# Performance work log

Hardware: AMD Instinct MI355X
Metric: run time of the kernel (lower is better)

Reference implementation:

```python
import jax, jax.numpy as jnp
import numpy as np

H, HK, D = 16, 4, 128          # query heads, kv heads, head_dim
HID, INTER = 2048, 8192        # hidden_size, intermediate_size
L, N_UND = 4096, 3072          # total packed len (sum(sample_lens)), num und tokens
SAMPLE_LENS = [2048, 2048]
EPS = 1e-6


def rmsnorm(x, w, eps=EPS):
    v = jnp.mean(jnp.square(x), axis=-1, keepdims=True)
    return x * jax.lax.rsqrt(v + eps) * w


def setup_inputs() -> dict:
    key = jax.random.key(0)
    ks = jax.random.split(key, 12)
    x = jax.random.normal(ks[0], (N_UND, HID), jnp.float32)
    und_idx = jnp.sort(jax.random.permutation(ks[1], L)[:N_UND]).astype(jnp.int64)
    # RoPE tables (source computes RoPE but its attention consumes pre-RoPE tensors)
    pos = jnp.arange(L, dtype=jnp.float32)
    inv_freq = 1.0 / (10000.0 ** (jnp.arange(0, D, 2, dtype=jnp.float32) / D))
    ang = pos[:, None] * inv_freq[None, :]
    cos = jnp.concatenate([jnp.cos(ang), jnp.cos(ang)], axis=-1)
    sin = jnp.concatenate([jnp.sin(ang), jnp.sin(ang)], axis=-1)
    # block-diagonal causal mask over packed sequence (one causal block per sample)
    offs = np.cumsum([0] + SAMPLE_LENS)
    m = np.zeros((L, L), dtype=bool)
    for a, b in zip(offs[:-1], offs[1:]):
        m[a:b, a:b] = np.tril(np.ones((b - a, b - a), dtype=bool))
    mask = jnp.asarray(m)
    w = lambda k, shape: jax.random.normal(k, shape, jnp.float32) * 0.02
    return dict(
        packed_sequence=x, und_idx=und_idx, cos=cos, sin=sin, mask=mask,
        Wq=w(ks[2], (H * D, HID)), bq=w(ks[3], (H * D,)),
        Wk=w(ks[4], (HK * D, HID)), bk=w(ks[5], (HK * D,)),
        Wv=w(ks[6], (HK * D, HID)), bv=w(ks[7], (HK * D,)),
        Wo=w(ks[8], (HID, H * D)),
        q_norm_w=jnp.ones((D,), jnp.float32), k_norm_w=jnp.ones((D,), jnp.float32),
        ln1_w=jnp.ones((HID,), jnp.float32), ln2_w=jnp.ones((HID,), jnp.float32),
        Wg=w(ks[9], (INTER, HID)), Wu=w(ks[10], (INTER, HID)), Wd=w(ks[11], (HID, INTER)),
    )


def reference(packed_sequence, und_idx, cos, sin, mask, Wq, bq, Wk, bk, Wv, bv, Wo,
              q_norm_w, k_norm_w, ln1_w, ln2_w, Wg, Wu, Wd):
    G = H // HK  # num_key_value_groups
    resid = packed_sequence
    x = rmsnorm(packed_sequence, ln1_w)
    # projections on und tokens only, then scatter into zero-initialized packed tensors
    q = (x @ Wq.T + bq).reshape(-1, H, D)
    k = (x @ Wk.T + bk).reshape(-1, HK, D)
    v = (x @ Wv.T + bv).reshape(-1, HK, D)
    Q = jnp.zeros((L, H, D), x.dtype).at[und_idx].set(q)
    K = jnp.zeros((L, HK, D), x.dtype).at[und_idx].set(k)
    V = jnp.zeros((L, HK, D), x.dtype).at[und_idx].set(v)
    # QK RMSNorm (zero rows stay zero, matching scatter-of-normed-und-rows)
    Q = rmsnorm(Q, q_norm_w)
    K = rmsnorm(K, k_norm_w)
    # NOTE: the source applies apply_rotary_pos_emb(Q, K, cos, sin) but both attention
    # branches consume the pre-RoPE normed tensors, so RoPE has no effect; we mirror that.
    Kx = jnp.repeat(K, G, axis=1)  # [L, H, D] GQA expand (each kv head repeated G times)
    Vx = jnp.repeat(V, G, axis=1)
    scores = jnp.einsum('qhd,khd->hqk', Q, Kx) / jnp.sqrt(jnp.asarray(D, x.dtype))
    scores = jnp.where(mask[None], scores, jnp.finfo(scores.dtype).min)
    attn = jax.nn.softmax(scores, axis=-1)
    ctx = jnp.einsum('hqk,khd->qhd', attn, Vx).reshape(L, H * D)
    attn_out = ctx[und_idx] @ Wo.T
    h = resid + attn_out
    y = rmsnorm(h, ln2_w)
    mlp = (jax.nn.silu(y @ Wg.T) * (y @ Wu.T)) @ Wd.T
    return h + mlp
```

## Files before the change

### kernel.cpp

```cpp
#include <hip/hip_runtime.h>
#include <math.h>


#define NU     3072
#define LPACK  4096
#define HIDN   2048
#define QKV_LD 3072
#define EPSF   1e-6f

typedef unsigned short u16;
typedef unsigned int   u32;
typedef unsigned long long u64;
typedef __attribute__((ext_vector_type(8)))  __bf16 bf16x8;
typedef __attribute__((ext_vector_type(4)))  float  f32x4;
typedef __attribute__((ext_vector_type(16))) float  f32x16;

union FRAG { uint4 q; u16 u[8]; bf16x8 b; };

__device__ __forceinline__ u16 f2bf(float f) {
    u32 u = __float_as_uint(f);
    u32 r = (u + 0x7fffu + ((u >> 16) & 1u)) >> 16;
    return (u16)r;
}
__device__ __forceinline__ float bf2f(u16 h) {
    return __uint_as_float(((u32)h) << 16);
}
__device__ __forceinline__ void gload_lds16(const u16* g, u16* lds) {
    __builtin_amdgcn_global_load_lds(
        (const __attribute__((address_space(1))) u32*)g,
        (__attribute__((address_space(3))) u32*)lds, 16, 0, 0);
}


__global__ __launch_bounds__(256) void inv_init_kernel(int* __restrict__ inv) {
    inv[blockIdx.x * 256 + threadIdx.x] = -1;
}
__global__ __launch_bounds__(256) void inv_set_kernel(const int* __restrict__ und,
                                                      int* __restrict__ inv) {
    int i = blockIdx.x * 256 + threadIdx.x;
    inv[und[i]] = i;
}


struct CvtArgs {
    const float* src[7];
    u16*         dst[7];
    int          n8[7];
};

__global__ __launch_bounds__(256) void cvt_all_kernel(CvtArgs a) {
    int seg = blockIdx.y;
    const float* in = a.src[seg];
    u16* out = a.dst[seg];
    int n8 = a.n8[seg];
    int idx = blockIdx.x * 256 + threadIdx.x;
    int stride = gridDim.x * 256;
    for (int i = idx; i < n8; i += stride) {
        float4 va = *(const float4*)(in + (size_t)i * 8);
        float4 vb = *(const float4*)(in + (size_t)i * 8 + 4);
        FRAG f;
        f.u[0] = f2bf(va.x); f.u[1] = f2bf(va.y); f.u[2] = f2bf(va.z); f.u[3] = f2bf(va.w);
        f.u[4] = f2bf(vb.x); f.u[5] = f2bf(vb.y); f.u[6] = f2bf(vb.z); f.u[7] = f2bf(vb.w);
        *(uint4*)(out + (size_t)i * 8) = f.q;
    }
}


__global__ __launch_bounds__(256) void rmsnorm_bf16_kernel(const float* __restrict__ in,
                                                           const float* __restrict__ w,
                                                           u16* __restrict__ out) {
    int row = blockIdx.x;
    const float4* p = (const float4*)(in + (size_t)row * HIDN);
    float4 a = p[threadIdx.x * 2];
    float4 b = p[threadIdx.x * 2 + 1];
    float ss = a.x*a.x + a.y*a.y + a.z*a.z + a.w*a.w
             + b.x*b.x + b.y*b.y + b.z*b.z + b.w*b.w;
    #pragma unroll
    for (int off = 32; off > 0; off >>= 1) ss += __shfl_xor(ss, off, 64);
    __shared__ float red[4];
    if ((threadIdx.x & 63) == 0) red[threadIdx.x >> 6] = ss;
    __syncthreads();
    float tot = red[0] + red[1] + red[2] + red[3];
    float sc  = rsqrtf(tot * (1.0f / HIDN) + EPSF);
    const float4* wp = (const float4*)w;
    float4 w0 = wp[threadIdx.x * 2], w1 = wp[threadIdx.x * 2 + 1];
    FRAG f;
    f.u[0] = f2bf(a.x*sc*w0.x); f.u[1] = f2bf(a.y*sc*w0.y);
    f.u[2] = f2bf(a.z*sc*w0.z); f.u[3] = f2bf(a.w*sc*w0.w);
    f.u[4] = f2bf(b.x*sc*w1.x); f.u[5] = f2bf(b.y*sc*w1.y);
    f.u[6] = f2bf(b.z*sc*w1.z); f.u[7] = f2bf(b.w*sc*w1.w);
    *(uint4*)(out + (size_t)row * HIDN + threadIdx.x * 8) = f.q;
}


__global__ __launch_bounds__(64) void qnorm_kernel(u16* __restrict__ qkv,
                                                   const float* __restrict__ w) {
    int i = blockIdx.x, h = blockIdx.y, t = threadIdx.x;
    u16* p = qkv + (size_t)i * QKV_LD + h * 128 + t * 2;
    u32 pr = *(u32*)p;
    float x0 = bf2f((u16)(pr & 0xffff)), x1 = bf2f((u16)(pr >> 16));
    float ss = x0*x0 + x1*x1;
    #pragma unroll
    for (int off = 32; off > 0; off >>= 1) ss += __shfl_xor(ss, off, 64);
    float sc = rsqrtf(ss * (1.0f / 128.f) + EPSF);
    float2 wv = *(const float2*)(w + t * 2);
    u32 res = (u32)f2bf(x0*sc*wv.x) | ((u32)f2bf(x1*sc*wv.y) << 16);
    *(u32*)p = res;
}


__global__ __launch_bounds__(64) void scatter_kv_kernel(const u16* __restrict__ qkvb,
                                                        const int* __restrict__ inv,
                                                        const float* __restrict__ knw,
                                                        u16* __restrict__ Kb,
                                                        u16* __restrict__ Vb) {
    int l = blockIdx.x, hkk = blockIdx.y, t = threadIdx.x;
    int i = inv[l];
    size_t off = (size_t)l * 512 + hkk * 128 + t * 2;
    if (i < 0) {
        *(u32*)(Kb + off) = 0u;
        *(u32*)(Vb + off) = 0u;
        return;
    }
    const u16* kp = qkvb + (size_t)i * QKV_LD + 2048 + hkk * 128 + t * 2;
    u32 kv = *(const u32*)kp;
    float k0 = bf2f((u16)(kv & 0xffff)), k1 = bf2f((u16)(kv >> 16));
    float ss = k0*k0 + k1*k1;
    #pragma unroll
    for (int off2 = 32; off2 > 0; off2 >>= 1) ss += __shfl_xor(ss, off2, 64);
    float sc = rsqrtf(ss * (1.0f / 128.f) + EPSF);
    float2 wv = *(const float2*)(knw + t * 2);
    u32 res = (u32)f2bf(k0*sc*wv.x) | ((u32)f2bf(k1*sc*wv.y) << 16);
    *(u32*)(Kb + off) = res;
    const u16* vp = qkvb + (size_t)i * QKV_LD + 2560 + hkk * 128 + t * 2;
    *(u32*)(Vb + off) = *(const u32*)vp;
}


template <int MODE>
__global__ __launch_bounds__(256, 2) void gemm_bf16_kernel(
        const u16* __restrict__ A, int lda,
        const u16* __restrict__ B0, const u16* __restrict__ B1, const u16* __restrict__ B2,
        int n1, int n2, int ldb,
        const float* __restrict__ bias0, const float* __restrict__ bias1,
        const float* __restrict__ bias2,
        const float* __restrict__ addend,
        void* __restrict__ Cout, int ldc, int K)
{
    __shared__ u16 As[2][128 * 64];
    __shared__ u16 Bs[2][128 * 64];
    const int tid = threadIdx.x;
    const int w = tid >> 6, lane = tid & 63;
    const int gx = gridDim.x;
    int id = blockIdx.y * gx + blockIdx.x;
    const int cpx = (gridDim.x * gridDim.y) >> 3;
    id = (id & 7) * cpx + (id >> 3);
    const int m0 = (id / gx) * 128, n0 = (id % gx) * 128;
    const u16* Bp; const float* bias; int nb;
    if (n0 < n1)      { Bp = B0; bias = bias0; nb = n0; }
    else if (n0 < n2) { Bp = B1; bias = bias1; nb = n0 - n1; }
    else              { Bp = B2; bias = bias2; nb = n0 - n2; }
    const int wr = w >> 1, wc = w & 1;
    const int cl = lane & 15, kg = lane >> 4;

    f32x4 acc[4][4];
    #pragma unroll
    for (int i = 0; i < 4; ++i)
        #pragma unroll
        for (int j = 0; j < 4; ++j)
            #pragma unroll
            for (int r = 0; r < 4; ++r) acc[i][j][r] = 0.f;

    const int NT = K >> 6;
    #pragma unroll
    for (int j = 0; j < 4; ++j) {
        int slot = j * 256 + tid;
        int row = slot >> 3, jp = slot & 7;
        int j2 = jp ^ (row & 7);
        gload_lds16(A + (size_t)(m0 + row) * lda + j2 * 8,
                    &As[0][(j * 256 + w * 64) * 8]);
        gload_lds16(Bp + (size_t)(nb + row) * ldb + j2 * 8,
                    &Bs[0][(j * 256 + w * 64) * 8]);
    }
    __syncthreads();

    for (int t = 0; t < NT; ++t) {
        const int cur = t & 1;
        if (t + 1 < NT) {
            int k0 = (t + 1) << 6;
            #pragma unroll
            for (int j = 0; j < 4; ++j) {
                int slot = j * 256 + tid;
                int row = slot >> 3, jp = slot & 7;
                int j2 = jp ^ (row & 7);
                gload_lds16(A + (size_t)(m0 + row) * lda + k0 + j2 * 8,
                            &As[cur ^ 1][(j * 256 + w * 64) * 8]);
                gload_lds16(Bp + (size_t)(nb + row) * ldb + k0 + j2 * 8,
                            &Bs[cur ^ 1][(j * 256 + w * 64) * 8]);
            }
        }
        #pragma unroll
        for (int ks = 0; ks < 2; ++ks) {
            FRAG af[4], bfr[4];
            #pragma unroll
            for (int mi = 0; mi < 4; ++mi) {
                int row = wr * 64 + mi * 16 + cl;
                int dblk = ks * 4 + kg;
                af[mi].q = *(const uint4*)&As[cur][row * 64 + ((dblk ^ (row & 7)) * 8)];
            }
            #pragma unroll
            for (int ni = 0; ni < 4; ++ni) {
                int row = wc * 64 + ni * 16 + cl;
                int dblk = ks * 4 + kg;
                bfr[ni].q = *(const uint4*)&Bs[cur][row * 64 + ((dblk ^ (row & 7)) * 8)];
            }
            #pragma unroll
            for (int mi = 0; mi < 4; ++mi)
                #pragma unroll
                for (int ni = 0; ni < 4; ++ni)
                    acc[mi][ni] = __builtin_amdgcn_mfma_f32_16x16x32_bf16(
                        af[mi].b, bfr[ni].b, acc[mi][ni], 0, 0, 0);
        }
        __syncthreads();
    }
    #pragma unroll
    for (int mi = 0; mi < 4; ++mi) {
        #pragma unroll
        for (int ni = 0; ni < 4; ++ni) {
            int gcol = n0 + wc * 64 + ni * 16 + cl;
            float bv = 0.f;
            if (MODE == 0) bv = bias[nb + wc * 64 + ni * 16 + cl];
            #pragma unroll
            for (int r = 0; r < 4; ++r) {
                int grow = m0 + wr * 64 + mi * 16 + kg * 4 + r;
                float v = acc[mi][ni][r] + bv;
                if (MODE == 0) {
                    ((u16*)Cout)[(size_t)grow * ldc + gcol] = f2bf(v);
                } else {
                    v += addend[(size_t)grow * ldc + gcol];
                    ((float*)Cout)[(size_t)grow * ldc + gcol] = v;
                }
            }
        }
    }
}


__global__ __launch_bounds__(256, 2) void gemm_gateup_bf16_kernel(
        const u16* __restrict__ A,
        const u16* __restrict__ Bg, const u16* __restrict__ Bu,
        u16* __restrict__ act, int ldc)
{
    __shared__ u16 As[2][128 * 32];
    __shared__ u16 Gs[2][128 * 32];
    __shared__ u16 Us[2][128 * 32];
    const int tid = threadIdx.x;
    const int w = tid >> 6, lane = tid & 63;
    const int gx = gridDim.x;
    int id = blockIdx.y * gx + blockIdx.x;
    const int cpx = (gridDim.x * gridDim.y) >> 3;
    id = (id & 7) * cpx + (id >> 3);
    const int m0 = (id / gx) * 128, n0 = (id % gx) * 128;
    const int wr = w >> 1, wc = w & 1;
    const int cl = lane & 15, kg = lane >> 4;

    f32x4 ag[4][4], au[4][4];
    #pragma unroll
    for (int i = 0; i < 4; ++i)
        #pragma unroll
        for (int j = 0; j < 4; ++j)
            #pragma unroll
            for (int r = 0; r < 4; ++r) { ag[i][j][r] = 0.f; au[i][j][r] = 0.f; }

    const int NT = HIDN >> 5;
    #pragma unroll
    for (int j = 0; j < 2; ++j) {
        int slot = j * 256 + tid;
        int row = slot >> 2, jp = slot & 3;
        int j2 = jp ^ (row & 3);
        gload_lds16(A + (size_t)(m0 + row) * HIDN + j2 * 8,
                    &As[0][(j * 256 + w * 64) * 8]);
        gload_lds16(Bg + (size_t)(n0 + row) * HIDN + j2 * 8,
                    &Gs[0][(j * 256 + w * 64) * 8]);
        gload_lds16(Bu + (size_t)(n0 + row) * HIDN + j2 * 8,
                    &Us[0][(j * 256 + w * 64) * 8]);
    }
    __syncthreads();

    for (int t = 0; t < NT; ++t) {
        const int cur = t & 1;
        if (t + 1 < NT) {
            int k0 = (t + 1) << 5;
            #pragma unroll
            for (int j = 0; j < 2; ++j) {
                int slot = j * 256 + tid;
                int row = slot >> 2, jp = slot & 3;
                int j2 = jp ^ (row & 3);
                gload_lds16(A + (size_t)(m0 + row) * HIDN + k0 + j2 * 8,
                            &As[cur ^ 1][(j * 256 + w * 64) * 8]);
                gload_lds16(Bg + (size_t)(n0 + row) * HIDN + k0 + j2 * 8,
                            &Gs[cur ^ 1][(j * 256 + w * 64) * 8]);
                gload_lds16(Bu + (size_t)(n0 + row) * HIDN + k0 + j2 * 8,
                            &Us[cur ^ 1][(j * 256 + w * 64) * 8]);
            }
        }
        {
            FRAG af[4], gf[4], uf[4];
            #pragma unroll
            for (int mi = 0; mi < 4; ++mi) {
                int row = wr * 64 + mi * 16 + cl;
                af[mi].q = *(const uint4*)&As[cur][row * 32 + ((kg ^ (row & 3)) * 8)];
            }
            #pragma unroll
            for (int ni = 0; ni < 4; ++ni) {
                int row = wc * 64 + ni * 16 + cl;
                gf[ni].q = *(const uint4*)&Gs[cur][row * 32 + ((kg ^ (row & 3)) * 8)];
                uf[ni].q = *(const uint4*)&Us[cur][row * 32 + ((kg ^ (row & 3)) * 8)];
            }
            #pragma unroll
            for (int mi = 0; mi < 4; ++mi)
                #pragma unroll
                for (int ni = 0; ni < 4; ++ni) {
                    ag[mi][ni] = __builtin_amdgcn_mfma_f32_16x16x32_bf16(
                        af[mi].b, gf[ni].b, ag[mi][ni], 0, 0, 0);
                    au[mi][ni] = __builtin_amdgcn_mfma_f32_16x16x32_bf16(
                        af[mi].b, uf[ni].b, au[mi][ni], 0, 0, 0);
                }
        }
        __syncthreads();
    }
    #pragma unroll
    for (int mi = 0; mi < 4; ++mi) {
        #pragma unroll
        for (int ni = 0; ni < 4; ++ni) {
            int gcol = n0 + wc * 64 + ni * 16 + cl;
            #pragma unroll
            for (int r = 0; r < 4; ++r) {
                int grow = m0 + wr * 64 + mi * 16 + kg * 4 + r;
                float g = ag[mi][ni][r], u = au[mi][ni][r];
                float s = g / (1.f + __expf(-g));
                act[(size_t)grow * ldc + gcol] = f2bf(s * u);
            }
        }
    }
}


__global__ __launch_bounds__(256, 2) void attn_mfma_kernel(
        const u16* __restrict__ qkv,
        const u16* __restrict__ Kb,
        const u16* __restrict__ Vb,
        const int* __restrict__ und,
        u16* __restrict__ ctxb)
{
    int id = blockIdx.y * 24 + blockIdx.x;
    id = (id & 7) * 48 + (id >> 3);
    const int h = id / 24, hk = h >> 2;
    const int i0 = (id % 24) * 128;
    const int tid = threadIdx.x;
    const int w = tid >> 6, lane = tid & 63;
    const int ql = lane & 31, hi = lane >> 5;

    __shared__ __align__(16) unsigned char SM[36864];
    u16*  Kt = (u16*)SM;
    u16*  Vt = (u16*)(SM + 16384);
    float* Ot = (float*)SM;

    const int iq  = i0 + w * 32 + ql;
    const int pqv = und[iq];
    const int rsv = pqv & ~2047;
    const int kend_w = __shfl(pqv, 31, 64);
    const int kbeg_w = __shfl(pqv, 0, 64) & ~2047;
    const int kbeg_b = und[i0] & ~2047;
    const int kend_b = und[i0 + 127];
    const int nt = ((kend_b - kbeg_b) >> 5) + 1;

    FRAG qf[8];
    const u16* qbase = qkv + (size_t)iq * QKV_LD + h * 128;
    #pragma unroll
    for (int ds = 0; ds < 8; ++ds)
        qf[ds].q = *(const uint4*)(qbase + ds * 16 + hi * 8);

    f32x16 Oa[4];
    #pragma unroll
    for (int dg = 0; dg < 4; ++dg)
        #pragma unroll
        for (int r = 0; r < 16; ++r) Oa[dg][r] = 0.f;
    float m_run = -1e30f, l_run = 0.f;
    const float SCALE = 0.08838834764831845f;

    const int r2 = tid >> 4, c = tid & 15;

    FRAG vr0, vr1;
    {
        #pragma unroll
        for (int j = 0; j < 2; ++j) {
            int sb = (j * 4 + w) * 64;
            int slot = sb + lane;
            int r = slot >> 4, jp = slot & 15;
            int jj = jp ^ (r & 15);
            gload_lds16(Kb + (size_t)(kbeg_b + r) * 512 + hk * 128 + jj * 8,
                        &Kt[sb * 8]);
        }
        const u16* v0 = Vb + (size_t)(kbeg_b + 2 * r2) * 512 + hk * 128 + c * 8;
        vr0.q = *(const uint4*)v0;
        vr1.q = *(const uint4*)(v0 + 512);
    }

    for (int t = 0; t < nt; ++t) {
        const int cur = t & 1;
        const int k0 = kbeg_b + t * 32;
        #pragma unroll
        for (int i = 0; i < 8; ++i) {
            u32 val = (u32)vr0.u[i] | ((u32)vr1.u[i] << 16);
            *(u32*)&Vt[cur * 4608 + (c * 8 + i) * 36 + r2 * 2] = val;
        }
        __syncthreads();
        if (t + 1 < nt) {
            int kn = k0 + 32;
            #pragma unroll
            for (int j = 0; j < 2; ++j) {
                int sb = (j * 4 + w) * 64;
                int slot = sb + lane;
                int r = slot >> 4, jp = slot & 15;
                int jj = jp ^ (r & 15);
                gload_lds16(Kb + (size_t)(kn + r) * 512 + hk * 128 + jj * 8,
                            &Kt[(cur ^ 1) * 4096 + sb * 8]);
            }
            const u16* v0 = Vb + (size_t)(kn + 2 * r2) * 512 + hk * 128 + c * 8;
            vr0.q = *(const uint4*)v0;
            vr1.q = *(const uint4*)(v0 + 512);
        }
        if (k0 + 31 >= kbeg_w && k0 <= kend_w) {
            f32x16 st;
            #pragma unroll
            for (int r = 0; r < 16; ++r) st[r] = 0.f;
            __builtin_amdgcn_s_setprio(1);
            #pragma unroll
            for (int ds = 0; ds < 8; ++ds) {
                FRAG kf;
                kf.q = *(const uint4*)&Kt[cur * 4096 + ql * 128 +
                                          (((ds * 2 + hi) ^ (ql & 15)) * 8)];
                st = __builtin_amdgcn_mfma_f32_32x32x16_bf16(kf.b, qf[ds].b, st, 0, 0, 0);
            }
            __builtin_amdgcn_s_setprio(0);
            int kh4 = k0 + (hi << 2);
            #pragma unroll
            for (int r = 0; r < 16; ++r) {
                int key = kh4 + (r & 3) + ((r >> 2) << 3);
                st[r] = (key >= rsv && key <= pqv) ? st[r] * SCALE : -1e30f;
            }
            float ma = fmaxf(fmaxf(st[0], st[1]), fmaxf(st[2], st[3]));
            float mb = fmaxf(fmaxf(st[4], st[5]), fmaxf(st[6], st[7]));
            float mc = fmaxf(fmaxf(st[8], st[9]), fmaxf(st[10], st[11]));
            float md = fmaxf(fmaxf(st[12], st[13]), fmaxf(st[14], st[15]));
            float mloc = fmaxf(fmaxf(ma, mb), fmaxf(mc, md));
            float mfull = fmaxf(mloc, __shfl_xor(mloc, 32, 64));
            float mnew = fmaxf(m_run, mfull);
            float corr = __expf(m_run - mnew);
            #pragma unroll
            for (int r = 0; r < 16; ++r)
                st[r] = (st[r] > -1e29f) ? __expf(st[r] - mnew) : 0.f;
            float sa = (st[0] + st[1]) + (st[2] + st[3]);
            float sb2 = (st[4] + st[5]) + (st[6] + st[7]);
            float sc2 = (st[8] + st[9]) + (st[10] + st[11]);
            float sd = (st[12] + st[13]) + (st[14] + st[15]);
            float psum = (sa + sb2) + (sc2 + sd);
            psum += __shfl_xor(psum, 32, 64);
            l_run = l_run * corr + psum;
            if (__any(mnew > m_run)) {
                #pragma unroll
                for (int r = 0; r < 16; ++r) {
                    float cr = __shfl(corr, (r & 3) + ((r >> 2) << 3) + (hi << 2), 64);
                    #pragma unroll
                    for (int dg = 0; dg < 4; ++dg) Oa[dg][r] *= cr;
                }
            }
            m_run = mnew;
            u32 pa[2][4];
            #pragma unroll
            for (int s = 0; s < 2; ++s) {
                #pragma unroll
                for (int t2 = 0; t2 < 2; ++t2) {
                    u32 a, b;
                    asm volatile("v_cvt_pk_bf16_f32 %0, %1, %2"
                                 : "=v"(a) : "v"(st[8*s + 2*t2]), "v"(st[8*s + 2*t2 + 1]));
                    asm volatile("v_cvt_pk_bf16_f32 %0, %1, %2"
                                 : "=v"(b) : "v"(st[8*s + 4 + 2*t2]), "v"(st[8*s + 4 + 2*t2 + 1]));
                    asm volatile("v_permlane32_swap_b32 %0, %1" : "+v"(a), "+v"(b));
                    pa[s][t2] = a; pa[s][t2 + 2] = b;
                }
            }
            __builtin_amdgcn_s_setprio(1);
            #pragma unroll
            for (int s = 0; s < 2; ++s) {
                FRAG pau;
                pau.q = make_uint4(pa[s][0], pa[s][1], pa[s][2], pa[s][3]);
                #pragma unroll
                for (int dg = 0; dg < 4; ++dg) {
                    FRAG vfr;
                    const u16* vp = &Vt[cur * 4608 + (dg * 32 + ql) * 36 +
                                        s * 16 + hi * 8];
                    *(u64*)&vfr.u[0] = *(const u64*)vp;
                    *(u64*)&vfr.u[4] = *(const u64*)(vp + 4);
                    Oa[dg] = __builtin_amdgcn_mfma_f32_32x32x16_bf16(
                        pau.b, vfr.b, Oa[dg], 0, 0, 0);
                }
            }
            __builtin_amdgcn_s_setprio(0);
        }
    }
    __syncthreads();

    float linv = 1.f / l_run;
    #pragma unroll
    for (int dg = 0; dg < 4; ++dg) {
        #pragma unroll
        for (int r = 0; r < 16; ++r)
            Ot[w * 1152 + ((r & 3) + ((r >> 2) << 3) + (hi << 2)) * 36 + ql] = Oa[dg][r];
        __syncthreads();
        float4 v0 = *(const float4*)&Ot[w * 1152 + ql * 36 + hi * 16 + 0];
        float4 v1 = *(const float4*)&Ot[w * 1152 + ql * 36 + hi * 16 + 4];
        float4 v2 = *(const float4*)&Ot[w * 1152 + ql * 36 + hi * 16 + 8];
        float4 v3 = *(const float4*)&Ot[w * 1152 + ql * 36 + hi * 16 + 12];
        FRAG a, b;
        a.u[0] = f2bf(v0.x * linv); a.u[1] = f2bf(v0.y * linv);
        a.u[2] = f2bf(v0.z * linv); a.u[3] = f2bf(v0.w * linv);
        a.u[4] = f2bf(v1.x * linv); a.u[5] = f2bf(v1.y * linv);
        a.u[6] = f2bf(v1.z * linv); a.u[7] = f2bf(v1.w * linv);
        b.u[0] = f2bf(v2.x * linv); b.u[1] = f2bf(v2.y * linv);
        b.u[2] = f2bf(v2.z * linv); b.u[3] = f2bf(v2.w * linv);
        b.u[4] = f2bf(v3.x * linv); b.u[5] = f2bf(v3.y * linv);
        b.u[6] = f2bf(v3.z * linv); b.u[7] = f2bf(v3.w * linv);
        u16* dst = ctxb + (size_t)(i0 + w * 32 + ql) * HIDN + h * 128 + dg * 32 + hi * 16;
        *(uint4*)dst = a.q;
        *(uint4*)(dst + 8) = b.q;
        __syncthreads();
    }
}


extern "C" void kernel_launch(void* const* d_in, const int* in_sizes, int n_in,
                              void* d_out, int out_size, void* d_ws, size_t ws_size,
                              hipStream_t stream) {
    const float* x    = (const float*)d_in[0];
    const int*   und  = (const int*)d_in[1];
    const float* Wq  = (const float*)d_in[5];
    const float* bq  = (const float*)d_in[6];
    const float* Wk  = (const float*)d_in[7];
    const float* bk  = (const float*)d_in[8];
    const float* Wv  = (const float*)d_in[9];
    const float* bv  = (const float*)d_in[10];
    const float* Wo  = (const float*)d_in[11];
    const float* qnw = (const float*)d_in[12];
    const float* knw = (const float*)d_in[13];
    const float* ln1 = (const float*)d_in[14];
    const float* ln2 = (const float*)d_in[15];
    const float* Wg  = (const float*)d_in[16];
    const float* Wu  = (const float*)d_in[17];
    const float* Wd  = (const float*)d_in[18];
    float* out = (float*)d_out;

    char* W = (char*)d_ws;
    u16* WqB = (u16*)(W + 0);
    u16* WkB = (u16*)(W + 8388608);
    u16* WvB = (u16*)(W + 10485760);
    u16* WoB = (u16*)(W + 12582912);
    u16* WgB = (u16*)(W + 20971520);
    u16* WuB = (u16*)(W + 54525952);
    u16* WdB = (u16*)(W + 88080384);
    char* R1 = W + 121634816;
    u16* qkvb = (u16*)R1;
    u16* ctxb = (u16*)(R1 + 18874368);
    u16* acth = (u16*)R1;
    float* hbuf = (float*)(W + 153092096);
    u16* xnb = (u16*)(W + 178257920);
    u16* Kbf = xnb;
    u16* Vbf = (u16*)(W + 178257920 + 4194304);
    u16* ynb = xnb;
    int* inv = (int*)(W + 190840832);

    const int BIG = 1 << 30;

    inv_init_kernel<<<16, 256, 0, stream>>>(inv);
    inv_set_kernel<<<12, 256, 0, stream>>>(und, inv);

    CvtArgs ca;
    ca.src[0] = Wq; ca.dst[0] = WqB; ca.n8[0] = 524288;
    ca.src[1] = Wk; ca.dst[1] = WkB; ca.n8[1] = 131072;
    ca.src[2] = Wv; ca.dst[2] = WvB; ca.n8[2] = 131072;
    ca.src[3] = Wo; ca.dst[3] = WoB; ca.n8[3] = 524288;
    ca.src[4] = Wg; ca.dst[4] = WgB; ca.n8[4] = 2097152;
    ca.src[5] = Wu; ca.dst[5] = WuB; ca.n8[5] = 2097152;
    ca.src[6] = Wd; ca.dst[6] = WdB; ca.n8[6] = 2097152;
    cvt_all_kernel<<<dim3(1024, 7), 256, 0, stream>>>(ca);

    rmsnorm_bf16_kernel<<<NU, 256, 0, stream>>>(x, ln1, xnb);
    gemm_bf16_kernel<0><<<dim3(24, 24), 256, 0, stream>>>(
        xnb, 2048, WqB, WkB, WvB, 2048, 2560, 2048,
        bq, bk, bv, nullptr, qkvb, QKV_LD, 2048);
    qnorm_kernel<<<dim3(NU, 16), 64, 0, stream>>>(qkvb, qnw);
    scatter_kv_kernel<<<dim3(LPACK, 4), 64, 0, stream>>>(qkvb, inv, knw, Kbf, Vbf);
    attn_mfma_kernel<<<dim3(24, 16), 256, 0, stream>>>(qkvb, Kbf, Vbf, und, ctxb);
    gemm_bf16_kernel<1><<<dim3(16, 24), 256, 0, stream>>>(
        ctxb, 2048, WoB, WoB, WoB, BIG, BIG, 2048,
        nullptr, nullptr, nullptr, x, hbuf, 2048, 2048);
    rmsnorm_bf16_kernel<<<NU, 256, 0, stream>>>(hbuf, ln2, ynb);
    gemm_gateup_bf16_kernel<<<dim3(32, 24), 256, 0, stream>>>(
        ynb, WgB, WuB, acth, 4096);
    gemm_bf16_kernel<1><<<dim3(16, 24), 256, 0, stream>>>(
        acth, 4096, WdB, WdB, WdB, BIG, BIG, 8192,
        nullptr, nullptr, nullptr, hbuf, out, 2048, 4096);
    gemm_gateup_bf16_kernel<<<dim3(32, 24), 256, 0, stream>>>(
        ynb, WgB + (size_t)4096 * 2048, WuB + (size_t)4096 * 2048, acth, 4096);
    gemm_bf16_kernel<1><<<dim3(16, 24), 256, 0, stream>>>(
        acth, 4096, WdB + 4096, WdB, WdB, BIG, BIG, 8192,
        nullptr, nullptr, nullptr, out, out, 2048, 4096);
}
```

Baseline: 831.7 us.

## Single-buffer generic GEMM LDS tiles and change gate/up swizzle pattern

The generic bf16 GEMM drops its double-buffered LDS prefetch for a single buffer. Each k-step now loads A and B, syncs, then computes, which halves LDS use and may allow more resident blocks. The cost is that global loads no longer overlap MFMA compute. Separately, the gate/up GEMM's XOR swizzle now uses (row>>1)&3 instead of row&3, meant to cut LDS bank conflicts for 64-byte rows.

```diff
diff --git a/kernel.cpp b/kernel.cpp
--- a/kernel.cpp
+++ b/kernel.cpp
@@ -147,8 +147,8 @@
         const float* __restrict__ addend,
         void* __restrict__ Cout, int ldc, int K)
 {
-    __shared__ u16 As[2][128 * 64];
-    __shared__ u16 Bs[2][128 * 64];
+    __shared__ u16 As[128 * 64];
+    __shared__ u16 Bs[128 * 64];
     const int tid = threadIdx.x;
     const int w = tid >> 6, lane = tid & 63;
     const int gx = gridDim.x;
@@ -171,34 +171,24 @@
             #pragma unroll
             for (int r = 0; r < 4; ++r) acc[i][j][r] = 0.f;
 
-    const int NT = K >> 6;
-    #pragma unroll
-    for (int j = 0; j < 4; ++j) {
-        int slot = j * 256 + tid;
-        int row = slot >> 3, jp = slot & 7;
-        int j2 = jp ^ (row & 7);
-        gload_lds16(A + (size_t)(m0 + row) * lda + j2 * 8,
-                    &As[0][(j * 256 + w * 64) * 8]);
-        gload_lds16(Bp + (size_t)(nb + row) * ldb + j2 * 8,
-                    &Bs[0][(j * 256 + w * 64) * 8]);
-    }
-    __syncthreads();
-
-    for (int t = 0; t < NT; ++t) {
-        const int cur = t & 1;
-        if (t + 1 < NT) {
-            int k0 = (t + 1) << 6;
-            #pragma unroll
-            for (int j = 0; j < 4; ++j) {
-                int slot = j * 256 + tid;
-                int row = slot >> 3, jp = slot & 7;
-                int j2 = jp ^ (row & 7);
-                gload_lds16(A + (size_t)(m0 + row) * lda + k0 + j2 * 8,
-                            &As[cur ^ 1][(j * 256 + w * 64) * 8]);
-                gload_lds16(Bp + (size_t)(nb + row) * ldb + k0 + j2 * 8,
-                            &Bs[cur ^ 1][(j * 256 + w * 64) * 8]);
-            }
-        }
+    for (int k0 = 0; k0 < K; k0 += 64) {
+        #pragma unroll
+        for (int j = 0; j < 4; ++j) {
+            int slot = j * 256 + tid;
+            int row = slot >> 3, jp = slot & 7;
+            int j2 = jp ^ (row & 7);
+            gload_lds16(A + (size_t)(m0 + row) * lda + k0 + j2 * 8,
+                        &As[(j * 256 + w * 64) * 8]);
+        }
+        #pragma unroll
+        for (int j = 0; j < 4; ++j) {
+            int slot = j * 256 + tid;
+            int row = slot >> 3, jp = slot & 7;
+            int j2 = jp ^ (row & 7);
+            gload_lds16(Bp + (size_t)(nb + row) * ldb + k0 + j2 * 8,
+                        &Bs[(j * 256 + w * 64) * 8]);
+        }
+        __syncthreads();
         #pragma unroll
         for (int ks = 0; ks < 2; ++ks) {
             FRAG af[4], bfr[4];
@@ -206,13 +196,13 @@
             for (int mi = 0; mi < 4; ++mi) {
                 int row = wr * 64 + mi * 16 + cl;
                 int dblk = ks * 4 + kg;
-                af[mi].q = *(const uint4*)&As[cur][row * 64 + ((dblk ^ (row & 7)) * 8)];
+                af[mi].q = *(const uint4*)&As[row * 64 + ((dblk ^ (row & 7)) * 8)];
             }
             #pragma unroll
             for (int ni = 0; ni < 4; ++ni) {
                 int row = wc * 64 + ni * 16 + cl;
                 int dblk = ks * 4 + kg;
-                bfr[ni].q = *(const uint4*)&Bs[cur][row * 64 + ((dblk ^ (row & 7)) * 8)];
+                bfr[ni].q = *(const uint4*)&Bs[row * 64 + ((dblk ^ (row & 7)) * 8)];
             }
             #pragma unroll
             for (int mi = 0; mi < 4; ++mi)
@@ -277,7 +267,7 @@
     for (int j = 0; j < 2; ++j) {
         int slot = j * 256 + tid;
         int row = slot >> 2, jp = slot & 3;
-        int j2 = jp ^ (row & 3);
+        int j2 = jp ^ ((row >> 1) & 3);
         gload_lds16(A + (size_t)(m0 + row) * HIDN + j2 * 8,
                     &As[0][(j * 256 + w * 64) * 8]);
         gload_lds16(Bg + (size_t)(n0 + row) * HIDN + j2 * 8,
@@ -295,7 +285,7 @@
             for (int j = 0; j < 2; ++j) {
                 int slot = j * 256 + tid;
                 int row = slot >> 2, jp = slot & 3;
-                int j2 = jp ^ (row & 3);
+                int j2 = jp ^ ((row >> 1) & 3);
                 gload_lds16(A + (size_t)(m0 + row) * HIDN + k0 + j2 * 8,
                             &As[cur ^ 1][(j * 256 + w * 64) * 8]);
                 gload_lds16(Bg + (size_t)(n0 + row) * HIDN + k0 + j2 * 8,
@@ -309,13 +299,13 @@
             #pragma unroll
             for (int mi = 0; mi < 4; ++mi) {
                 int row = wr * 64 + mi * 16 + cl;
-                af[mi].q = *(const uint4*)&As[cur][row * 32 + ((kg ^ (row & 3)) * 8)];
+                af[mi].q = *(const uint4*)&As[cur][row * 32 + ((kg ^ ((row >> 1) & 3)) * 8)];
             }
             #pragma unroll
             for (int ni = 0; ni < 4; ++ni) {
                 int row = wc * 64 + ni * 16 + cl;
-                gf[ni].q = *(const uint4*)&Gs[cur][row * 32 + ((kg ^ (row & 3)) * 8)];
-                uf[ni].q = *(const uint4*)&Us[cur][row * 32 + ((kg ^ (row & 3)) * 8)];
+                gf[ni].q = *(const uint4*)&Gs[cur][row * 32 + ((kg ^ ((row >> 1) & 3)) * 8)];
+                uf[ni].q = *(const uint4*)&Us[cur][row * 32 + ((kg ^ ((row >> 1) & 3)) * 8)];
             }
             #pragma unroll
             for (int mi = 0; mi < 4; ++mi)
```

New measurement: 799.0 us. 3.9% less time.
